# Performance work log

Measured on AMD Instinct MI355X. Metric: run time of the kernel, lower is better.

The kernel has to match this reference:

```python
import math
import jax, jax.numpy as jnp
import numpy as np

N_LAYER = 4
D = 192        # n_embd
NH = 4         # n_head
N = 3072       # n_neurons = n_embd * mlp_dim_mult // n_head
VOCAB = 256
BLOCK = 4096
EPS = 1e-5
B, T = 1, 1024


def get_freqs(n, theta=2.0 ** 16):
    t = np.arange(n, dtype=np.float32)
    q = np.floor(t / 2.0) * 2.0  # quantize(t, 2)
    return (1.0 / theta ** (q / n) / (2.0 * math.pi)).astype(np.float32)

_FREQS = jnp.asarray(get_freqs(N))  # [N]


def _ln(x):
    # LayerNorm over last dim, no affine (elementwise_affine=False)
    m = jnp.mean(x, axis=-1, keepdims=True)
    v = jnp.var(x, axis=-1, keepdims=True)
    return (x - m) / jnp.sqrt(v + EPS)


def _rope(x):
    # x: [B, nh, T, N]
    t = x.shape[2]
    phases = (jnp.arange(t, dtype=jnp.float32)[:, None] * _FREQS[None, :]) % 1.0 * (2.0 * math.pi)  # [T, N]
    x_even = x[..., 0::2]
    x_odd = x[..., 1::2]
    v_rot = jnp.stack((-x_odd, x_even), axis=-1).reshape(x.shape)
    return x * jnp.cos(phases) + v_rot * jnp.sin(phases)


def setup_inputs() -> dict:
    key = jax.random.key(0)
    ks = jax.random.split(key, 7)
    s = 0.02
    return {
        "idx": jax.random.randint(ks[0], (B, T), 0, VOCAB, dtype=jnp.int64)
        if jax.config.jax_enable_x64 else jax.random.randint(ks[0], (B, T), 0, VOCAB, dtype=jnp.int32),
        "decoder_x": jax.random.normal(ks[1], (NH, D, N), jnp.float32) * s,
        "decoder_y": jax.random.normal(ks[2], (NH, D, N), jnp.float32) * s,
        "encoder": jax.random.normal(ks[3], (NH * N, D), jnp.float32) * s,
        "embed": jax.random.normal(ks[4], (VOCAB, D), jnp.float32) * s,
        "pos_emb": jax.random.normal(ks[5], (BLOCK, D), jnp.float32) * s,
        "lm_head": jax.random.normal(ks[6], (D, VOCAB), jnp.float32) * s,
    }


def reference(idx, decoder_x, decoder_y, encoder, embed, pos_emb, lm_head):
    b, t = idx.shape
    x = embed[idx] + pos_emb[:t][None]          # [B, T, D]
    x = _ln(x)
    mask = jnp.tril(jnp.ones((t, t), jnp.float32), k=-1)  # strictly lower
    for _ in range(N_LAYER):
        # encoder-side sparsification: D -> N per head
        x_sparse = jax.nn.relu(jnp.einsum('btd,hdn->bhtn', x, decoder_x))  # [B,nh,T,N]
        qr = _rope(x_sparse)
        scores = jnp.einsum('bhtn,bhsn->bhts', qr, qr) * mask              # [B,nh,T,T]
        ykv = _ln(jnp.einsum('bhts,bsd->bhtd', scores, x))                 # [B,nh,T,D]
        y_sparse = jax.nn.relu(jnp.einsum('bhtd,hdn->bhtn', ykv, decoder_y))
        xy = x_sparse * y_sparse                                           # [B,nh,T,N]
        # [B,T,nh*N] @ [nh*N, D]
        ymlp = jnp.einsum('bhtn,hnd->btd', xy, encoder.reshape(NH, N, D))
        x = _ln(x + _ln(ymlp))
    logits = jnp.einsum('btd,dv->btv', x, lm_head)                         # [B,T,vocab]
    return logits
```

## Files before the change

kernel.cpp:

```cpp
#include <hip/hip_runtime.h>
#include <hip/hip_bf16.h>

using bf16 = __hip_bfloat16;

#define D_DIM   192
#define N_DIM   3072
#define NHEAD   4
#define T_SEQ   1024
#define HN      12288
#define NP2     1536
#define VOCABSZ 256
#define NLAYER  4
#define LN_EPS  1e-5f
#define TWO_PI  6.2831853071795864f

typedef __attribute__((ext_vector_type(8)))  short          s16x8;
typedef __attribute__((ext_vector_type(8)))  unsigned short u16x8;
typedef __attribute__((ext_vector_type(4)))  float          f32x4;
typedef __attribute__((ext_vector_type(16))) float          f32x16;

__device__ __forceinline__ float b2f(bf16 v) { return __bfloat162float(v); }
__device__ __forceinline__ float us2f(unsigned short u) {
    unsigned int x = ((unsigned int)u) << 16;
    return __builtin_bit_cast(float, x);
}
__device__ __forceinline__ unsigned short f2us(float f) {
    bf16 b = __float2bfloat16(f);
    return __builtin_bit_cast(unsigned short, b);
}

__global__ void fill_out(float* __restrict__ out, float val, int nelem) {
    int i = blockIdx.x * 256 + threadIdx.x;
    if (i < nelem) out[i] = val;
}

__global__ void t_cvt(const float* __restrict__ in, bf16* __restrict__ out,
                      int R, int C, long inZ, long outZ) {
    __shared__ float tile[64][65];
    in  += inZ  * blockIdx.z;
    out += outZ * blockIdx.z;
    const int tx = threadIdx.x & 63, ty = threadIdx.x >> 6;
    const int r0 = blockIdx.y * 64, c0 = blockIdx.x * 64;
    #pragma unroll
    for (int rr = 0; rr < 16; rr++) {
        int row = ty * 16 + rr;
        tile[row][tx] = in[(size_t)(r0 + row) * C + c0 + tx];
    }
    __syncthreads();
    #pragma unroll
    for (int rr = 0; rr < 16; rr++) {
        int row = ty * 16 + rr;
        out[(size_t)(c0 + row) * R + r0 + tx] = __float2bfloat16(tile[tx][row]);
    }
}

__device__ __forceinline__ void wave_sum2(float& s, float& ss) {
    #pragma unroll
    for (int off = 1; off < 64; off <<= 1) {
        s  += __shfl_xor(s,  off, 64);
        ss += __shfl_xor(ss, off, 64);
    }
}

__global__ void k_embed(const int* __restrict__ idx, const float* __restrict__ emb,
                        const float* __restrict__ pos, float* __restrict__ x,
                        bf16* __restrict__ xb) {
    int t = blockIdx.x, l = threadIdx.x;
    int tok = idx[t];
    const float* e = emb + tok * D_DIM;
    const float* p = pos + t * D_DIM;
    float v0 = e[l] + p[l], v1 = e[l + 64] + p[l + 64], v2 = e[l + 128] + p[l + 128];
    float s = v0 + v1 + v2, ss = v0 * v0 + v1 * v1 + v2 * v2;
    wave_sum2(s, ss);
    float m = s / D_DIM, r = rsqrtf(ss / D_DIM - m * m + LN_EPS);
    float* xr = x + t * D_DIM;
    bf16*  xo = xb + (size_t)t * D_DIM;
    float o0 = (v0 - m) * r, o1 = (v1 - m) * r, o2 = (v2 - m) * r;
    xr[l] = o0; xr[l + 64] = o1; xr[l + 128] = o2;
    xo[l] = __float2bfloat16(o0);
    xo[l + 64] = __float2bfloat16(o1);
    xo[l + 128] = __float2bfloat16(o2);
}

__global__ void k_ln(float* __restrict__ buf) {
    int l = threadIdx.x;
    float* row = buf + (size_t)blockIdx.x * D_DIM;
    float v0 = row[l], v1 = row[l + 64], v2 = row[l + 128];
    float s = v0 + v1 + v2, ss = v0 * v0 + v1 * v1 + v2 * v2;
    wave_sum2(s, ss);
    float m = s / D_DIM, r = rsqrtf(ss / D_DIM - m * m + LN_EPS);
    row[l] = (v0 - m) * r; row[l + 64] = (v1 - m) * r; row[l + 128] = (v2 - m) * r;
}

__global__ void k_ln2b(const float* __restrict__ P0, const float* __restrict__ P1,
                       bf16* __restrict__ outb) {
    int l = threadIdx.x;
    size_t off = (size_t)blockIdx.x * D_DIM;
    const float* r0 = P0 + off;
    const float* r1 = P1 + off;
    float v0 = r0[l] + r1[l];
    float v1 = r0[l + 64] + r1[l + 64];
    float v2 = r0[l + 128] + r1[l + 128];
    float s = v0 + v1 + v2, ss = v0 * v0 + v1 * v1 + v2 * v2;
    wave_sum2(s, ss);
    float m = s / D_DIM, r = rsqrtf(ss / D_DIM - m * m + LN_EPS);
    bf16* o = outb + off;
    o[l]       = __float2bfloat16((v0 - m) * r);
    o[l + 64]  = __float2bfloat16((v1 - m) * r);
    o[l + 128] = __float2bfloat16((v2 - m) * r);
}

template <int NSLAB>
__global__ void k_resid(float* __restrict__ x, const float* __restrict__ P,
                        bf16* __restrict__ xb) {
    int l = threadIdx.x, t = blockIdx.x;
    float y0 = 0.f, y1 = 0.f, y2 = 0.f;
    #pragma unroll
    for (int p = 0; p < NSLAB; p++) {
        const float* r = P + (size_t)p * T_SEQ * D_DIM + (size_t)t * D_DIM;
        y0 += r[l]; y1 += r[l + 64]; y2 += r[l + 128];
    }
    float* xr = x + (size_t)t * D_DIM;
    float s = y0 + y1 + y2, ss = y0 * y0 + y1 * y1 + y2 * y2;
    wave_sum2(s, ss);
    float m1 = s / D_DIM, r1 = rsqrtf(ss / D_DIM - m1 * m1 + LN_EPS);
    float v0 = xr[l] + (y0 - m1) * r1;
    float v1 = xr[l + 64] + (y1 - m1) * r1;
    float v2 = xr[l + 128] + (y2 - m1) * r1;
    s = v0 + v1 + v2; ss = v0 * v0 + v1 * v1 + v2 * v2;
    wave_sum2(s, ss);
    float m2 = s / D_DIM, r2 = rsqrtf(ss / D_DIM - m2 * m2 + LN_EPS);
    float o0 = (v0 - m2) * r2, o1 = (v1 - m2) * r2, o2 = (v2 - m2) * r2;
    xr[l] = o0; xr[l + 64] = o1; xr[l + 128] = o2;
    bf16* xo = xb + (size_t)t * D_DIM;
    xo[l] = __float2bfloat16(o0);
    xo[l + 64] = __float2bfloat16(o1);
    xo[l + 128] = __float2bfloat16(o2);
}

__global__ void k_tables(ushort2* __restrict__ csT) {
    int gid = blockIdx.x * 256 + threadIdx.x;
    int t = gid / NP2, p = gid % NP2;
    float qf = (float)(2 * p);
    float f = exp2f(qf * (-16.0f / 3072.0f)) * (1.0f / (float)TWO_PI);
    float ph = fmodf((float)t * f, 1.0f) * (float)TWO_PI;
    ushort2 cs;
    cs.x = f2us(cosf(ph));
    cs.y = f2us(sinf(ph));
    csT[gid] = cs;
}

__launch_bounds__(256, 4)
__global__ void scores64(const bf16* __restrict__ qr, bf16* __restrict__ sc,
                         bf16* __restrict__ dbuf) {
    const int h  = blockIdx.z;
    const int kh = blockIdx.y;
    const int orig = blockIdx.x;
    const int L = (orig & 7) * 17 + (orig >> 3);
    int i = 0;
    while (((i + 1) * (i + 2)) >> 1 <= L) ++i;
    int j = L - ((i * (i + 1)) >> 1);
    const int t0 = i * 64, s0 = j * 64;
    const bool diag = (i == j);

    int arow = t0, brow = s0;
    if (kh == 1 && !diag) { arow = s0; brow = t0; }

    __shared__ short As[2][64][72];
    __shared__ short Bs[2][64][72];

    const int tid = threadIdx.x;
    const int lane = tid & 63, w = tid >> 6;
    const int wtm = (w >> 1) * 32, wtn = (w & 1) * 32;
    const int l31 = lane & 31, lhi = lane >> 5;
    const int r0 = tid >> 2;
    const int kq = (tid & 3) * 16;

    const int kBeg = kh * (N_DIM / 2);
    const bf16* gA = qr + (size_t)(arow + r0) * HN + h * N_DIM + kBeg + kq;
    const bf16* gB = qr + (size_t)(brow + r0) * HN + h * N_DIM + kBeg + kq;

    u16x8 pa0, pa1, pb0, pb1;
    u16x8 qa0, qa1, qb0, qb1;
    auto load0 = [&](int k0) {
        pa0 = *(const u16x8*)(gA + k0);
        pa1 = *(const u16x8*)(gA + k0 + 8);
        pb0 = *(const u16x8*)(gB + k0);
        pb1 = *(const u16x8*)(gB + k0 + 8);
    };
    auto load1 = [&](int k0) {
        qa0 = *(const u16x8*)(gA + k0);
        qa1 = *(const u16x8*)(gA + k0 + 8);
        qb0 = *(const u16x8*)(gB + k0);
        qb1 = *(const u16x8*)(gB + k0 + 8);
    };
    auto dep0 = [&](int buf) {
        *(u16x8*)&As[buf][r0][kq]     = pa0;
        *(u16x8*)&As[buf][r0][kq + 8] = pa1;
        *(u16x8*)&Bs[buf][r0][kq]     = pb0;
        *(u16x8*)&Bs[buf][r0][kq + 8] = pb1;
    };
    auto dep1 = [&](int buf) {
        *(u16x8*)&As[buf][r0][kq]     = qa0;
        *(u16x8*)&As[buf][r0][kq + 8] = qa1;
        *(u16x8*)&Bs[buf][r0][kq]     = qb0;
        *(u16x8*)&Bs[buf][r0][kq + 8] = qb1;
    };

    f32x16 acc;
    #pragma unroll
    for (int r = 0; r < 16; r++) acc[r] = 0.f;

    auto mfma_step = [&](int buf) {
        #pragma unroll
        for (int ks = 0; ks < 4; ks++) {
            s16x8 a = *(const s16x8*)&As[buf][wtm + l31][ks * 16 + lhi * 8];
            s16x8 b = *(const s16x8*)&Bs[buf][wtn + l31][ks * 16 + lhi * 8];
            acc = __builtin_amdgcn_mfma_f32_32x32x16_bf16(a, b, acc, 0, 0, 0);
        }
    };

    const int NIT = (N_DIM / 2) / 64;
    load0(0);
    load1(64);
    dep0(0);
    __syncthreads();

    for (int k = 0; k < NIT; k += 2) {
        if (k + 2 < NIT) load0((k + 2) * 64);
        mfma_step(0);
        if (k + 1 < NIT) dep1(1);
        __syncthreads();
        if (k + 1 < NIT) {
            if (k + 3 < NIT) load1((k + 3) * 64);
            mfma_step(1);
            if (k + 2 < NIT) dep0(0);
            __syncthreads();
        }
    }

    __syncthreads();
    short (*S)[72] = (short(*)[72])&As[0][0][0];
    const bool trS = (kh == 1) && !diag;
    #pragma unroll
    for (int r = 0; r < 16; r++) {
        int rr = wtm + (r & 3) + 8 * (r >> 2) + 4 * lhi;
        int cc = wtn + l31;
        float v = acc[r];
        if (diag && cc >= rr) v = 0.f;
        if (trS) S[cc][rr] = (short)f2us(v);
        else     S[rr][cc] = (short)f2us(v);
    }
    __syncthreads();
    if (kh == 1 && diag) {
        bf16* P = dbuf + (size_t)(h * 16 + i) * 4096;
        #pragma unroll
        for (int e = 0; e < 2; e++) {
            int idxe = tid + e * 256;
            int row = idxe >> 3, cg = (idxe & 7) * 8;
            u16x8 v = *(const u16x8*)&S[row][cg];
            *(u16x8*)(P + row * 64 + cg) = v;
        }
    } else {
        bf16* C = sc + (size_t)h * T_SEQ * T_SEQ;
        #pragma unroll
        for (int e = 0; e < 2; e++) {
            int idxe = tid + e * 256;
            int row = idxe >> 3, cg = (idxe & 7) * 8;
            u16x8 v = *(const u16x8*)&S[row][cg];
            *(u16x8*)(C + (size_t)(arow + row) * T_SEQ + brow + cg) = v;
        }
    }
}

__device__ __forceinline__ void stage_rope8(short* dst, const bf16* src,
                                            const ushort2* csP) {
    u16x8 v  = *(const u16x8*)src;
    u16x8 cs = *(const u16x8*)csP;
    u16x8 o;
    #pragma unroll
    for (int i = 0; i < 4; i++) {
        float e  = us2f(v[2 * i]), od = us2f(v[2 * i + 1]);
        float c  = us2f(cs[2 * i]), s = us2f(cs[2 * i + 1]);
        o[2 * i]     = f2us(e * c - od * s);
        o[2 * i + 1] = f2us(od * c + e * s);
    }
    *(u16x8*)dst = o;
}

__launch_bounds__(256)
__global__ void scores_fused(const bf16* __restrict__ xs,
                             const ushort2* __restrict__ csT,
                             bf16* __restrict__ sc) {
    const int h  = blockIdx.z;
    const int s0 = blockIdx.x * 64, t0 = blockIdx.y * 64;
    if (s0 > t0) return;
    __shared__ short As[64][40];
    __shared__ short Bs[64][40];
    const int tid  = threadIdx.x;
    const int srow = tid >> 2, kq = (tid & 3) * 8;
    const int lane = tid & 63, w = tid >> 6, qd = lane >> 4, lc = lane & 15;
    const int tA = t0 + srow, tB = s0 + srow;
    const bf16* gA = xs + (size_t)tA * HN + h * N_DIM + kq;
    const bf16* gB = xs + (size_t)tB * HN + h * N_DIM + kq;
    const ushort2* cA = csT + (size_t)tA * NP2 + (kq >> 1);
    const ushort2* cB = csT + (size_t)tB * NP2 + (kq >> 1);
    f32x4 acc[4] = {{0.f,0.f,0.f,0.f},{0.f,0.f,0.f,0.f},
                    {0.f,0.f,0.f,0.f},{0.f,0.f,0.f,0.f}};
    for (int k0 = 0; k0 < N_DIM; k0 += 32) {
        stage_rope8(&As[srow][kq], gA + k0, cA + (k0 >> 1));
        stage_rope8(&Bs[srow][kq], gB + k0, cB + (k0 >> 1));
        __syncthreads();
        s16x8 a = *(const s16x8*)&As[w * 16 + lc][qd * 8];
        #pragma unroll
        for (int j = 0; j < 4; j++) {
            s16x8 b = *(const s16x8*)&Bs[j * 16 + lc][qd * 8];
            acc[j] = __builtin_amdgcn_mfma_f32_16x16x32_bf16(a, b, acc[j], 0, 0, 0);
        }
        __syncthreads();
    }
    bf16* C = sc + (size_t)h * T_SEQ * T_SEQ;
    const bool diag = (s0 == t0);
    const int tbase = t0 + w * 16 + qd * 4;
    #pragma unroll
    for (int j = 0; j < 4; j++) {
        int s = s0 + j * 16 + lc;
        #pragma unroll
        for (int r = 0; r < 4; r++) {
            int t = tbase + r;
            C[(size_t)t * T_SEQ + s] =
                __float2bfloat16((!diag || s < t) ? acc[j][r] : 0.f);
        }
    }
}

template <int EPI, bool WQR, typename TA>
__launch_bounds__(256)
__global__ void dgemm128(const TA* __restrict__ A, const bf16* __restrict__ Bt,
                         bf16* __restrict__ xs, bf16* __restrict__ qr,
                         const ushort2* __restrict__ csT) {
    __shared__ __align__(16) short pool[2 * 2 * 128 * 40];
    short (*As)[128][40] = (short(*)[128][40])pool;
    short (*Bs)[128][40] = (short(*)[128][40])(pool + 2 * 128 * 40);

    const int tid = threadIdx.x;
    const int lane = tid & 63, w = tid >> 6;
    const int l31 = lane & 31, lhi = lane >> 5;
    const int wtm = (w >> 1) * 64, wtn = (w & 1) * 64;
    const int n0 = blockIdx.x * 128, m0 = blockIdx.y * 128;
    if constexpr (EPI == 2) A += (size_t)(n0 / N_DIM) * T_SEQ * D_DIM;

    const int r0 = tid >> 2, r1 = r0 + 64;
    const int kq = (tid & 3) * 8;

    const TA*   gA = A  + kq;
    const bf16* gB = Bt + kq;

    float4 fa00, fa01, fa02, fa03, fa10, fa11, fa12, fa13;
    u16x8 ba00, ba01, ba10, ba11;
    u16x8 pb00, pb01, pb10, pb11;
    auto load0 = [&](int k0) {
        if constexpr (__is_same(TA, float)) {
            const TA* a0 = gA + (size_t)(m0 + r0) * D_DIM + k0;
            const TA* a1 = gA + (size_t)(m0 + r1) * D_DIM + k0;
            fa00 = *(const float4*)a0; fa01 = *(const float4*)(a0 + 4);
            fa02 = *(const float4*)a1; fa03 = *(const float4*)(a1 + 4);
        } else {
            ba00 = *(const u16x8*)(gA + (size_t)(m0 + r0) * D_DIM + k0);
            ba01 = *(const u16x8*)(gA + (size_t)(m0 + r1) * D_DIM + k0);
        }
        pb00 = *(const u16x8*)(gB + (size_t)(n0 + r0) * D_DIM + k0);
        pb01 = *(const u16x8*)(gB + (size_t)(n0 + r1) * D_DIM + k0);
    };
    auto load1 = [&](int k0) {
        if constexpr (__is_same(TA, float)) {
            const TA* a0 = gA + (size_t)(m0 + r0) * D_DIM + k0;
            const TA* a1 = gA + (size_t)(m0 + r1) * D_DIM + k0;
            fa10 = *(const float4*)a0; fa11 = *(const float4*)(a0 + 4);
            fa12 = *(const float4*)a1; fa13 = *(const float4*)(a1 + 4);
        } else {
            ba10 = *(const u16x8*)(gA + (size_t)(m0 + r0) * D_DIM + k0);
            ba11 = *(const u16x8*)(gA + (size_t)(m0 + r1) * D_DIM + k0);
        }
        pb10 = *(const u16x8*)(gB + (size_t)(n0 + r0) * D_DIM + k0);
        pb11 = *(const u16x8*)(gB + (size_t)(n0 + r1) * D_DIM + k0);
    };
    auto dep0 = [&](int buf) {
        if constexpr (__is_same(TA, float)) {
            u16x8 o0, o1;
            o0[0] = f2us(fa00.x); o0[1] = f2us(fa00.y); o0[2] = f2us(fa00.z); o0[3] = f2us(fa00.w);
            o0[4] = f2us(fa01.x); o0[5] = f2us(fa01.y); o0[6] = f2us(fa01.z); o0[7] = f2us(fa01.w);
            o1[0] = f2us(fa02.x); o1[1] = f2us(fa02.y); o1[2] = f2us(fa02.z); o1[3] = f2us(fa02.w);
            o1[4] = f2us(fa03.x); o1[5] = f2us(fa03.y); o1[6] = f2us(fa03.z); o1[7] = f2us(fa03.w);
            *(u16x8*)&As[buf][r0][kq] = o0;
            *(u16x8*)&As[buf][r1][kq] = o1;
        } else {
            *(u16x8*)&As[buf][r0][kq] = ba00;
            *(u16x8*)&As[buf][r1][kq] = ba01;
        }
        *(u16x8*)&Bs[buf][r0][kq] = pb00;
        *(u16x8*)&Bs[buf][r1][kq] = pb01;
    };
    auto dep1 = [&](int buf) {
        if constexpr (__is_same(TA, float)) {
            u16x8 o0, o1;
            o0[0] = f2us(fa10.x); o0[1] = f2us(fa10.y); o0[2] = f2us(fa10.z); o0[3] = f2us(fa10.w);
            o0[4] = f2us(fa11.x); o0[5] = f2us(fa11.y); o0[6] = f2us(fa11.z); o0[7] = f2us(fa11.w);
            o1[0] = f2us(fa12.x); o1[1] = f2us(fa12.y); o1[2] = f2us(fa12.z); o1[3] = f2us(fa12.w);
            o1[4] = f2us(fa13.x); o1[5] = f2us(fa13.y); o1[6] = f2us(fa13.z); o1[7] = f2us(fa13.w);
            *(u16x8*)&As[buf][r0][kq] = o0;
            *(u16x8*)&As[buf][r1][kq] = o1;
        } else {
            *(u16x8*)&As[buf][r0][kq] = ba10;
            *(u16x8*)&As[buf][r1][kq] = ba11;
        }
        *(u16x8*)&Bs[buf][r0][kq] = pb10;
        *(u16x8*)&Bs[buf][r1][kq] = pb11;
    };

    f32x16 acc00, acc01, acc10, acc11;
    #pragma unroll
    for (int r = 0; r < 16; r++) { acc00[r] = 0.f; acc01[r] = 0.f; acc10[r] = 0.f; acc11[r] = 0.f; }

    auto mfma_step = [&](int buf) {
        #pragma unroll
        for (int ks = 0; ks < 2; ks++) {
            s16x8 a0 = *(const s16x8*)&As[buf][wtm + l31][ks * 16 + lhi * 8];
            s16x8 a1 = *(const s16x8*)&As[buf][wtm + 32 + l31][ks * 16 + lhi * 8];
            s16x8 b0 = *(const s16x8*)&Bs[buf][wtn + l31][ks * 16 + lhi * 8];
            s16x8 b1 = *(const s16x8*)&Bs[buf][wtn + 32 + l31][ks * 16 + lhi * 8];
            acc00 = __builtin_amdgcn_mfma_f32_32x32x16_bf16(a0, b0, acc00, 0, 0, 0);
            acc01 = __builtin_amdgcn_mfma_f32_32x32x16_bf16(a0, b1, acc01, 0, 0, 0);
            acc10 = __builtin_amdgcn_mfma_f32_32x32x16_bf16(a1, b0, acc10, 0, 0, 0);
            acc11 = __builtin_amdgcn_mfma_f32_32x32x16_bf16(a1, b1, acc11, 0, 0, 0);
        }
    };

    const int NIT = D_DIM / 32;
    load0(0);
    load1(32);
    dep0(0);
    __syncthreads();
    for (int k = 0; k < NIT; k += 2) {
        if (k + 2 < NIT) load0((k + 2) * 32);
        mfma_step(0);
        if (k + 1 < NIT) dep1(1);
        __syncthreads();
        if (k + 1 < NIT) {
            if (k + 3 < NIT) load1((k + 3) * 32);
            mfma_step(1);
            if (k + 2 < NIT) dep0(0);
            __syncthreads();
        }
    }

    short (*S)[136] = (short(*)[136])pool;
    #pragma unroll
    for (int r = 0; r < 16; r++) {
        int rb = (r & 3) + 8 * (r >> 2) + 4 * lhi;
        S[wtm + rb     ][wtn + l31     ] = (short)f2us(fmaxf(acc00[r], 0.f));
        S[wtm + rb     ][wtn + 32 + l31] = (short)f2us(fmaxf(acc01[r], 0.f));
        S[wtm + 32 + rb][wtn + l31     ] = (short)f2us(fmaxf(acc10[r], 0.f));
        S[wtm + 32 + rb][wtn + 32 + l31] = (short)f2us(fmaxf(acc11[r], 0.f));
    }
    __syncthreads();
    #pragma unroll
    for (int e = 0; e < 8; e++) {
        int idxe = tid + e * 256;
        int row = idxe >> 4, cg = idxe & 15;
        u16x8 v = *(const u16x8*)&S[row][cg * 8];
        int t = m0 + row, ngg = n0 + cg * 8;
        size_t ci = (size_t)t * HN + ngg;
        if constexpr (EPI == 1) {
            *(u16x8*)(xs + ci) = v;
            if constexpr (WQR) {
                int p0 = (ngg % N_DIM) >> 1;
                u16x8 cs8 = *(const u16x8*)&csT[(size_t)t * NP2 + p0];
                u16x8 o;
                #pragma unroll
                for (int q = 0; q < 4; q++) {
                    float ev = us2f(v[2 * q]), ov = us2f(v[2 * q + 1]);
                    float c = us2f(cs8[2 * q]), s = us2f(cs8[2 * q + 1]);
                    o[2 * q]     = f2us(ev * c - ov * s);
                    o[2 * q + 1] = f2us(ov * c + ev * s);
                }
                *(u16x8*)(qr + ci) = o;
            }
        } else {
            u16x8 g = *(const u16x8*)(xs + ci);
            u16x8 o;
            #pragma unroll
            for (int q = 0; q < 8; q++) o[q] = f2us(us2f(g[q]) * us2f(v[q]));
            *(u16x8*)(xs + ci) = o;
        }
    }
}

template <typename TA, int MODE>
__launch_bounds__(256)
__global__ void mfma_gemm(const TA* __restrict__ A, const bf16* __restrict__ Bt,
                          float* __restrict__ C, const bf16* __restrict__ aux,
                          int K, int kSeg, int lda, int ldb, int ldc,
                          long aZ, long bZ, long cZ) {
    constexpr bool DUAL = (MODE == 1);
    constexpr int TILES = DUAL ? 6 : 4;
    __shared__ __align__(16) short pool[TILES * 64 * 72];
    short (*As)[64][72] = (short(*)[64][72])pool;
    short (*Bs)[64][72] = (short(*)[64][72])(pool + 2 * 64 * 72);
    short (*Ms)[64][72] = (short(*)[64][72])(pool + 4 * 64 * 72);

    const int z = blockIdx.z;
    const int tid = threadIdx.x;
    const int n0 = blockIdx.x * 64, m0 = blockIdx.y * 64;
    const int srow = tid >> 2, sk = (tid & 3) * 16;
    const int lane = tid & 63, w = tid >> 6;
    const int l31 = lane & 31, lhi = lane >> 5;
    const int wm = (w >> 1) * 32, wn = (w & 1) * 32;

    int kBeg, kEnd, zh = 0;
    if constexpr (MODE == 1) {
        zh = z >> 1;
        const int seg = z & 1;
        A += aZ * zh;
        C += cZ * zh + bZ * seg;
        const int kc = (m0 + 64 < K) ? m0 + 64 : K;
        const int half0 = ((kc + 127) >> 7) << 6;
        kBeg = seg ? half0 : 0;
        kEnd = seg ? kc : half0;
    } else if constexpr (MODE == 2) {
        A += aZ * z; Bt += bZ * z; C += cZ * z;
        kBeg = z * kSeg; kEnd = kBeg + kSeg;
    } else if constexpr (MODE == 3) {
        A += aZ * z; Bt += bZ * z; C += cZ * z;
        kBeg = 0; kEnd = (m0 + 64 < K) ? m0 + 64 : K;
    } else {
        A += aZ * z; Bt += bZ * z; C += cZ * z;
        kBeg = 0; kEnd = K;
    }

    const TA*   ga = A  + (size_t)(m0 + srow) * lda + sk;
    const bf16* gb = Bt + (size_t)(n0 + srow) * ldb + sk;

    auto msrc = [&](int k0) -> const bf16* {
        if (k0 == m0)
            return aux + (size_t)(zh * 16 + (m0 >> 6)) * 4096
                       + (size_t)srow * 64 + sk;
        return (const bf16*)A + (size_t)(k0 + srow) * lda + m0 + sk;
    };

    float4 f00, f01, f02, f03, f10, f11, f12, f13;
    u16x8 pa00, pa01, pa10, pa11, pb00, pb01, pb10, pb11;
    u16x8 pm00, pm01, pm10, pm11;
    auto load0 = [&](int k0) {
        if constexpr (__is_same(TA, float)) {
            f00 = *(const float4*)(ga + k0);
            f01 = *(const float4*)(ga + k0 + 4);
            f02 = *(const float4*)(ga + k0 + 8);
            f03 = *(const float4*)(ga + k0 + 12);
        } else {
            pa00 = *(const u16x8*)(ga + k0);
            pa01 = *(const u16x8*)(ga + k0 + 8);
        }
        pb00 = *(const u16x8*)(gb + k0);
        pb01 = *(const u16x8*)(gb + k0 + 8);
        if constexpr (DUAL) {
            const bf16* ms = msrc(k0);
            pm00 = *(const u16x8*)ms;
            pm01 = *(const u16x8*)(ms + 8);
        }
    };
    auto load1 = [&](int k0) {
        if constexpr (__is_same(TA, float)) {
            f10 = *(const float4*)(ga + k0);
            f11 = *(const float4*)(ga + k0 + 4);
            f12 = *(const float4*)(ga + k0 + 8);
            f13 = *(const float4*)(ga + k0 + 12);
        } else {
            pa10 = *(const u16x8*)(ga + k0);
            pa11 = *(const u16x8*)(ga + k0 + 8);
        }
        pb10 = *(const u16x8*)(gb + k0);
        pb11 = *(const u16x8*)(gb + k0 + 8);
        if constexpr (DUAL) {
            const bf16* ms = msrc(k0);
            pm10 = *(const u16x8*)ms;
            pm11 = *(const u16x8*)(ms + 8);
        }
    };
    auto dep0 = [&](int buf) {
        if constexpr (__is_same(TA, float)) {
            u16x8 o0, o1;
            o0[0] = f2us(f00.x); o0[1] = f2us(f00.y); o0[2] = f2us(f00.z); o0[3] = f2us(f00.w);
            o0[4] = f2us(f01.x); o0[5] = f2us(f01.y); o0[6] = f2us(f01.z); o0[7] = f2us(f01.w);
            o1[0] = f2us(f02.x); o1[1] = f2us(f02.y); o1[2] = f2us(f02.z); o1[3] = f2us(f02.w);
            o1[4] = f2us(f03.x); o1[5] = f2us(f03.y); o1[6] = f2us(f03.z); o1[7] = f2us(f03.w);
            *(u16x8*)&As[buf][srow][sk]     = o0;
            *(u16x8*)&As[buf][srow][sk + 8] = o1;
        } else {
            *(u16x8*)&As[buf][srow][sk]     = pa00;
            *(u16x8*)&As[buf][srow][sk + 8] = pa01;
        }
        *(u16x8*)&Bs[buf][srow][sk]     = pb00;
        *(u16x8*)&Bs[buf][srow][sk + 8] = pb01;
        if constexpr (DUAL) {
            *(u16x8*)&Ms[buf][srow][sk]     = pm00;
            *(u16x8*)&Ms[buf][srow][sk + 8] = pm01;
        }
    };
    auto dep1 = [&](int buf) {
        if constexpr (__is_same(TA, float)) {
            u16x8 o0, o1;
            o0[0] = f2us(f10.x); o0[1] = f2us(f10.y); o0[2] = f2us(f10.z); o0[3] = f2us(f10.w);
            o0[4] = f2us(f11.x); o0[5] = f2us(f11.y); o0[6] = f2us(f11.z); o0[7] = f2us(f11.w);
            o1[0] = f2us(f12.x); o1[1] = f2us(f12.y); o1[2] = f2us(f12.z); o1[3] = f2us(f12.w);
            o1[4] = f2us(f13.x); o1[5] = f2us(f13.y); o1[6] = f2us(f13.z); o1[7] = f2us(f13.w);
            *(u16x8*)&As[buf][srow][sk]     = o0;
            *(u16x8*)&As[buf][srow][sk + 8] = o1;
        } else {
            *(u16x8*)&As[buf][srow][sk]     = pa10;
            *(u16x8*)&As[buf][srow][sk + 8] = pa11;
        }
        *(u16x8*)&Bs[buf][srow][sk]     = pb10;
        *(u16x8*)&Bs[buf][srow][sk + 8] = pb11;
        if constexpr (DUAL) {
            *(u16x8*)&Ms[buf][srow][sk]     = pm10;
            *(u16x8*)&Ms[buf][srow][sk + 8] = pm11;
        }
    };

    f32x16 acc;
    #pragma unroll
    for (int r = 0; r < 16; r++) acc[r] = 0.f;

    auto mfma_step = [&](int buf) {
        #pragma unroll
        for (int ks = 0; ks < 4; ks++) {
            s16x8 a = *(const s16x8*)&As[buf][wm + l31][ks * 16 + lhi * 8];
            s16x8 b = *(const s16x8*)&Bs[buf][wn + l31][ks * 16 + lhi * 8];
            acc = __builtin_amdgcn_mfma_f32_32x32x16_bf16(a, b, acc, 0, 0, 0);
            if constexpr (DUAL) {
                s16x8 m2 = *(const s16x8*)&Ms[buf][wm + l31][ks * 16 + lhi * 8];
                acc = __builtin_amdgcn_mfma_f32_32x32x16_bf16(m2, b, acc, 0, 0, 0);
            }
        }
    };

    const int NIT = (kEnd - kBeg) >> 6;
    load0(kBeg);
    load1(kBeg + 64);
    dep0(0);
    __syncthreads();

    for (int k = 0; k < NIT; k += 2) {
        if (k + 2 < NIT) load0(kBeg + (k + 2) * 64);
        mfma_step(0);
        if (k + 1 < NIT) dep1(1);
        __syncthreads();
        if (k + 1 < NIT) {
            if (k + 3 < NIT) load1(kBeg + (k + 3) * 64);
            mfma_step(1);
            if (k + 2 < NIT) dep0(0);
            __syncthreads();
        }
    }

    #pragma unroll
    for (int r = 0; r < 16; r++) {
        int row = m0 + wm + (r & 3) + 8 * (r >> 2) + 4 * lhi;
        int col = n0 + wn + l31;
        C[(size_t)row * ldc + col] = acc[r];
    }
}

extern "C" void kernel_launch(void* const* d_in, const int* in_sizes, int n_in,
                              void* d_out, int out_size, void* d_ws, size_t ws_size,
                              hipStream_t stream) {
    const int*   idx   = (const int*)  d_in[0];
    const float* dec_x = (const float*)d_in[1];
    const float* dec_y = (const float*)d_in[2];
    const float* enc   = (const float*)d_in[3];
    const float* emb   = (const float*)d_in[4];
    const float* pose  = (const float*)d_in[5];
    const float* lmh   = (const float*)d_in[6];
    float* out = (float*)d_out;

    char* wp = (char*)d_ws;
    float*   x    = (float*)wp;              wp += (size_t)T_SEQ * D_DIM * 4;
    bf16*    xs   = (bf16*)wp;               wp += (size_t)T_SEQ * HN * 2;
    ushort2* csT  = (ushort2*)wp;            wp += (size_t)T_SEQ * NP2 * 4;
    bf16*    sc   = (bf16*)wp;               wp += (size_t)NHEAD * T_SEQ * T_SEQ * 2;
    float*   ykv  = (float*)wp;              wp += (size_t)NHEAD * T_SEQ * D_DIM * 4;
    float*   ymlp = (float*)wp;              wp += (size_t)T_SEQ * D_DIM * 4;
    bf16*    xT   = (bf16*)wp;               wp += (size_t)D_DIM * T_SEQ * 2;
    bf16*    wX   = (bf16*)wp;               wp += (size_t)NHEAD * N_DIM * D_DIM * 2;
    bf16*    wY   = (bf16*)wp;               wp += (size_t)NHEAD * N_DIM * D_DIM * 2;
    bf16*    wE   = (bf16*)wp;               wp += (size_t)D_DIM * HN * 2;
    bf16*    wL   = (bf16*)wp;               wp += (size_t)VOCABSZ * D_DIM * 2;
    const size_t BASE_NEED = (size_t)(wp - (char*)d_ws);
    bf16*    qr   = (bf16*)wp;
    const size_t FULL_NEED = BASE_NEED + (size_t)T_SEQ * HN * 2;
    bf16*  dbuf  = (bf16*)ymlp;

    if (ws_size < BASE_NEED) {
        fill_out<<<(out_size + 255) / 256, 256, 0, stream>>>(out, (float)ws_size, out_size);
        return;
    }
    const bool USE_QR = (ws_size >= FULL_NEED);

    bf16*  xb_main = (bf16*)sc;
    bf16*  xb_fb   = (bf16*)ymlp;
    float* ymlpP16 = (float*)qr;
    bf16*  ykvb    = (bf16*)((char*)qr + (size_t)16 * T_SEQ * D_DIM * 4);
    float* ymlpP8  = (float*)sc;

    bf16* xb = USE_QR ? xb_main : xb_fb;

    t_cvt<<<dim3(48, 3, 4), 256, 0, stream>>>(dec_x, wX, D_DIM, N_DIM,
                                              (long)D_DIM * N_DIM, (long)N_DIM * D_DIM);
    t_cvt<<<dim3(48, 3, 4), 256, 0, stream>>>(dec_y, wY, D_DIM, N_DIM,
                                              (long)D_DIM * N_DIM, (long)N_DIM * D_DIM);
    t_cvt<<<dim3(3, 192, 1), 256, 0, stream>>>(enc, wE, HN, D_DIM, 0L, 0L);
    t_cvt<<<dim3(4, 3, 1), 256, 0, stream>>>(lmh, wL, D_DIM, VOCABSZ, 0L, 0L);

    k_tables<<<(T_SEQ * NP2) / 256, 256, 0, stream>>>(csT);
    k_embed<<<T_SEQ, 64, 0, stream>>>(idx, emb, pose, x, xb);

    for (int l = 0; l < NLAYER; ++l) {
        t_cvt<<<dim3(3, 16, 1), 256, 0, stream>>>(x, xT, T_SEQ, D_DIM, 0L, 0L);
        if (USE_QR) {
            dgemm128<1, true, bf16><<<dim3(96, 8), 256, 0, stream>>>(xb, wX, xs, qr, csT);
            scores64<<<dim3(136, 2, NHEAD), 256, 0, stream>>>(qr, sc, dbuf);
            long segZ = (long)((float*)qr - ykv);
            mfma_gemm<bf16, 1><<<dim3(3, 16, NHEAD * 2), 256, 0, stream>>>(
                sc, xT, ykv, dbuf, T_SEQ, 0, T_SEQ, T_SEQ, D_DIM,
                (long)T_SEQ * T_SEQ, segZ, (long)T_SEQ * D_DIM);
            k_ln2b<<<NHEAD * T_SEQ, 64, 0, stream>>>(ykv, (const float*)qr, ykvb);
            dgemm128<2, false, bf16><<<dim3(96, 8), 256, 0, stream>>>(
                ykvb, wY, xs, nullptr, nullptr);
            mfma_gemm<bf16, 2><<<dim3(3, 16, 16), 256, 0, stream>>>(
                xs, wE, ymlpP16, nullptr, HN, HN / 16, HN, HN, D_DIM,
                0L, 0L, (long)T_SEQ * D_DIM);
            k_resid<16><<<T_SEQ, 64, 0, stream>>>(x, ymlpP16, xb);
        } else {
            dgemm128<1, false, bf16><<<dim3(96, 8), 256, 0, stream>>>(xb, wX, xs, qr, csT);
            scores_fused<<<dim3(16, 16, NHEAD), 256, 0, stream>>>(xs, csT, sc);
            mfma_gemm<bf16, 3><<<dim3(3, 16, NHEAD), 256, 0, stream>>>(
                sc, xT, ykv, nullptr, T_SEQ, 0, T_SEQ, T_SEQ, D_DIM,
                (long)T_SEQ * T_SEQ, 0L, (long)T_SEQ * D_DIM);
            k_ln<<<NHEAD * T_SEQ, 64, 0, stream>>>(ykv);
            dgemm128<2, false, float><<<dim3(96, 8), 256, 0, stream>>>(
                ykv, wY, xs, nullptr, nullptr);
            mfma_gemm<bf16, 2><<<dim3(3, 16, 8), 256, 0, stream>>>(
                xs, wE, ymlpP8, nullptr, HN, HN / 8, HN, HN, D_DIM,
                0L, 0L, (long)T_SEQ * D_DIM);
            k_resid<8><<<T_SEQ, 64, 0, stream>>>(x, ymlpP8, xb);
        }
    }

    mfma_gemm<float, 0><<<dim3(4, 16, 1), 256, 0, stream>>>(
        x, wL, out, nullptr, D_DIM, 0, D_DIM, D_DIM, VOCABSZ, 0L, 0L, 0L);
}
```

Measured before the change: 519.2 us.

## Fuse decoder_y GEMM, gating product and encoder GEMM into one kernel

Replaces the separate y_sparse GEMM (which wrote the gated xy back to the xs buffer) and the split-K encoder GEMM with a single kernel. Each block computes a 64-token by 64-neuron relu(ykv@decoder_y) tile in registers, multiplies it by x_sparse in shared memory, and immediately accumulates it into a 64x192 encoder output, writing 16 split-K partials. This removes a full T x 12288 bf16 write and reread of xs plus one launch. In exchange the grid is only 256 blocks with serialized chunks, there is no load/compute overlap, and the many syncthreads per chunk may underuse the GPU.

```diff
diff --git a/kernel.cpp b/kernel.cpp
--- a/kernel.cpp
+++ b/kernel.cpp
@@ -496,6 +496,121 @@
     }
 }
 
+__launch_bounds__(256, 2)
+__global__ void gate_ymlp(const bf16* __restrict__ ykvb, const bf16* __restrict__ wY,
+                          const bf16* __restrict__ xs, const bf16* __restrict__ wE,
+                          float* __restrict__ P) {
+    const int tb = blockIdx.x, s = blockIdx.y;
+    const int t0  = tb * 64;
+    const int h   = s >> 2;
+    const int ng0 = s * 768;
+    const int nh0 = (s & 3) * 768;
+
+    __shared__ __align__(16) short A1s[64][200];
+    __shared__ __align__(16) short Bsh[192][72];
+    __shared__ __align__(16) short xyA[64][72];
+    short (*B1)[200] = (short(*)[200])&Bsh[0][0];
+
+    const int tid = threadIdx.x;
+    const int lane = tid & 63, w = tid >> 6;
+    const int l31 = lane & 31, lhi = lane >> 5;
+    const int wm  = (w >> 1) * 32;
+    const int wn1 = (w & 1) * 32;
+    const int wn2 = (w & 1) * 96;
+
+    {
+        const bf16* src = ykvb + ((size_t)h * T_SEQ + t0 + (tid >> 2)) * D_DIM
+                        + (tid & 3) * 48;
+        #pragma unroll
+        for (int j = 0; j < 6; j++) {
+            u16x8 v = *(const u16x8*)(src + j * 8);
+            *(u16x8*)&A1s[tid >> 2][(tid & 3) * 48 + j * 8] = v;
+        }
+    }
+
+    f32x16 oc0, oc1, oc2;
+    #pragma unroll
+    for (int r = 0; r < 16; r++) { oc0[r] = 0.f; oc1[r] = 0.f; oc2[r] = 0.f; }
+
+    __syncthreads();
+
+    for (int c = 0; c < 12; c++) {
+        const int nc = c * 64;
+        {
+            const bf16* src = wY + ((size_t)h * N_DIM + nh0 + nc + (tid >> 2)) * D_DIM
+                            + (tid & 3) * 48;
+            #pragma unroll
+            for (int j = 0; j < 6; j++) {
+                u16x8 v = *(const u16x8*)(src + j * 8);
+                *(u16x8*)&B1[tid >> 2][(tid & 3) * 48 + j * 8] = v;
+            }
+        }
+        __syncthreads();
+        f32x16 ys;
+        #pragma unroll
+        for (int r = 0; r < 16; r++) ys[r] = 0.f;
+        #pragma unroll
+        for (int ks = 0; ks < 12; ks++) {
+            s16x8 a = *(const s16x8*)&A1s[wm + l31][ks * 16 + lhi * 8];
+            s16x8 b = *(const s16x8*)&B1[wn1 + l31][ks * 16 + lhi * 8];
+            ys = __builtin_amdgcn_mfma_f32_32x32x16_bf16(a, b, ys, 0, 0, 0);
+        }
+        __syncthreads();
+        #pragma unroll
+        for (int r = 0; r < 16; r++) {
+            int rr = wm + (r & 3) + 8 * (r >> 2) + 4 * lhi;
+            xyA[rr][wn1 + l31] = (short)f2us(fmaxf(ys[r], 0.f));
+        }
+        __syncthreads();
+        {
+            int row = tid >> 2, c0l = (tid & 3) * 16;
+            const bf16* sx = xs + (size_t)(t0 + row) * HN + ng0 + nc + c0l;
+            #pragma unroll
+            for (int e = 0; e < 2; e++) {
+                u16x8 g = *(const u16x8*)(sx + e * 8);
+                u16x8 y = *(const u16x8*)&xyA[row][c0l + e * 8];
+                u16x8 o;
+                #pragma unroll
+                for (int q = 0; q < 8; q++) o[q] = f2us(us2f(g[q]) * us2f(y[q]));
+                *(u16x8*)&xyA[row][c0l + e * 8] = o;
+            }
+        }
+        {
+            #pragma unroll
+            for (int j = 0; j < 3; j++) {
+                int d  = (tid >> 2) * 3 + j;
+                int cc = (tid & 3) * 16;
+                const bf16* src = wE + (size_t)d * HN + ng0 + nc + cc;
+                u16x8 v0 = *(const u16x8*)src;
+                u16x8 v1 = *(const u16x8*)(src + 8);
+                *(u16x8*)&Bsh[d][cc]     = v0;
+                *(u16x8*)&Bsh[d][cc + 8] = v1;
+            }
+        }
+        __syncthreads();
+        #pragma unroll
+        for (int ks = 0; ks < 4; ks++) {
+            s16x8 a  = *(const s16x8*)&xyA[wm + l31][ks * 16 + lhi * 8];
+            s16x8 b0 = *(const s16x8*)&Bsh[wn2 + l31     ][ks * 16 + lhi * 8];
+            s16x8 b1 = *(const s16x8*)&Bsh[wn2 + 32 + l31][ks * 16 + lhi * 8];
+            s16x8 b2 = *(const s16x8*)&Bsh[wn2 + 64 + l31][ks * 16 + lhi * 8];
+            oc0 = __builtin_amdgcn_mfma_f32_32x32x16_bf16(a, b0, oc0, 0, 0, 0);
+            oc1 = __builtin_amdgcn_mfma_f32_32x32x16_bf16(a, b1, oc1, 0, 0, 0);
+            oc2 = __builtin_amdgcn_mfma_f32_32x32x16_bf16(a, b2, oc2, 0, 0, 0);
+        }
+        __syncthreads();
+    }
+
+    float* O = P + (size_t)s * T_SEQ * D_DIM;
+    #pragma unroll
+    for (int r = 0; r < 16; r++) {
+        int rt = t0 + wm + (r & 3) + 8 * (r >> 2) + 4 * lhi;
+        O[(size_t)rt * D_DIM + wn2 +      l31] = oc0[r];
+        O[(size_t)rt * D_DIM + wn2 + 32 + l31] = oc1[r];
+        O[(size_t)rt * D_DIM + wn2 + 64 + l31] = oc2[r];
+    }
+}
+
 template <typename TA, int MODE>
 __launch_bounds__(256)
 __global__ void mfma_gemm(const TA* __restrict__ A, const bf16* __restrict__ Bt,
@@ -735,11 +850,7 @@
                 sc, xT, ykv, dbuf, T_SEQ, 0, T_SEQ, T_SEQ, D_DIM,
                 (long)T_SEQ * T_SEQ, segZ, (long)T_SEQ * D_DIM);
             k_ln2b<<<NHEAD * T_SEQ, 64, 0, stream>>>(ykv, (const float*)qr, ykvb);
-            dgemm128<2, false, bf16><<<dim3(96, 8), 256, 0, stream>>>(
-                ykvb, wY, xs, nullptr, nullptr);
-            mfma_gemm<bf16, 2><<<dim3(3, 16, 16), 256, 0, stream>>>(
-                xs, wE, ymlpP16, nullptr, HN, HN / 16, HN, HN, D_DIM,
-                0L, 0L, (long)T_SEQ * D_DIM);
+            gate_ymlp<<<dim3(16, 16), 256, 0, stream>>>(ykvb, wY, xs, wE, ymlpP16);
             k_resid<16><<<T_SEQ, 64, 0, stream>>>(x, ymlpP16, xb);
         } else {
             dgemm128<1, false, bf16><<<dim3(96, 8), 256, 0, stream>>>(xb, wX, xs, qr, csT);
```

Result: faster. 501.2 us (-3.5%).
